# Kernel optimization log

Hardware: AMD Instinct MI355X
Metric: run time of the kernel (lower is better)

The kernel has to match this reference:

```python
import jax, jax.numpy as jnp
import numpy as np

D_MODEL = 1024
N_HEADS = 16
D_HEAD = 64


def setup_inputs() -> dict:
    key = jax.random.key(0)
    ks = jax.random.split(key, 5)
    B, T = 2, 2048
    scale = 1.0 / np.sqrt(D_MODEL)
    x = jax.random.normal(ks[0], (B, T, D_MODEL), dtype=jnp.float32)
    Wq = jax.random.normal(ks[1], (N_HEADS * D_HEAD, D_MODEL), dtype=jnp.float32) * scale
    Wk = jax.random.normal(ks[2], (N_HEADS * D_HEAD, D_MODEL), dtype=jnp.float32) * scale
    Wv = jax.random.normal(ks[3], (N_HEADS * D_HEAD, D_MODEL), dtype=jnp.float32) * scale
    Wo = jax.random.normal(ks[4], (D_MODEL, N_HEADS * D_HEAD), dtype=jnp.float32) * scale
    return {"x": x, "Wq": Wq, "Wk": Wk, "Wv": Wv, "Wo": Wo}


def reference(x, Wq, Wk, Wv, Wo):
    B, T, D = x.shape
    # Linear(y = x @ W.T), then split heads: [B, H, T, d]
    def split_heads(y):
        return y.reshape(B, T, N_HEADS, D_HEAD).transpose(0, 2, 1, 3)
    q = split_heads(x @ Wq.T)
    k = split_heads(x @ Wk.T)
    v = split_heads(x @ Wv.T)
    scale = D_HEAD ** -0.5
    # Materialized [B, H, T, T] scores, as in the original module
    scores = jnp.einsum('bhtd,bhTd->bhtT', q, k) * scale
    attn = jax.nn.softmax(scores, axis=-1)
    y = jnp.einsum('bhtT,bhTd->bhtd', attn, v)
    y = y.transpose(0, 2, 1, 3).reshape(B, T, N_HEADS * D_HEAD)
    return y @ Wo.T
```

## Files before the change

kernel.cpp:

```cpp
#include <hip/hip_runtime.h>
#include <hip/hip_bf16.h>

typedef __attribute__((ext_vector_type(8))) short bf16x8;
typedef __attribute__((ext_vector_type(4))) float f32x4;
typedef unsigned short u16t;

#define DEVINL static __device__ __forceinline__

DEVINL u16t f2bf(float f) {
  union { __hip_bfloat16 h; u16t u; } cv;
  cv.h = __float2bfloat16(f);
  return cv.u;
}

DEVINL unsigned cvt_pk_bf16(float a, float b) {
  unsigned r;
  asm("v_cvt_pk_bf16_f32 %0, %1, %2" : "=v"(r) : "v"(a), "v"(b));
  return r;
}

DEVINL void async16(void* lds, const void* g) {
  __builtin_amdgcn_global_load_lds((const __attribute__((address_space(1))) void*)g,
                                   (__attribute__((address_space(3))) void*)lds,
                                   16, 0, 0);
}

__global__ __launch_bounds__(256) void convert_bf16(
    const float* __restrict__ x,  const float* __restrict__ wq,
    const float* __restrict__ wk, const float* __restrict__ wv,
    const float* __restrict__ wo,
    u16t* __restrict__ xb, u16t* __restrict__ wqb, u16t* __restrict__ wkb,
    u16t* __restrict__ wvb, u16t* __restrict__ wob) {
  const int blk = blockIdx.x;
  const float* src; u16t* dst; size_t off;
  if (blk < 4096)      { src = x;  dst = xb;  off = (size_t)blk * 1024; }
  else if (blk < 5120) { src = wq; dst = wqb; off = (size_t)(blk - 4096) * 1024; }
  else if (blk < 6144) { src = wk; dst = wkb; off = (size_t)(blk - 5120) * 1024; }
  else if (blk < 7168) { src = wv; dst = wvb; off = (size_t)(blk - 6144) * 1024; }
  else                 { src = wo; dst = wob; off = (size_t)(blk - 7168) * 1024; }
  const size_t i = off + (size_t)threadIdx.x * 4;
  const float4 v = *(const float4*)&src[i];
  ushort4 r;
  r.x = f2bf(v.x); r.y = f2bf(v.y); r.z = f2bf(v.z); r.w = f2bf(v.w);
  *(ushort4*)&dst[i] = r;
}

template <int MODE, int BM>
__global__ __launch_bounds__(256) void gemm_bt(
    const u16t* __restrict__ A, const u16t* __restrict__ B,
    void* __restrict__ C0, void* __restrict__ C1, void* __restrict__ C2,
    int M, int N, int K) {
  constexpr int MI = BM / 32;
  __shared__ u16t As[2][BM * 32];
  __shared__ u16t Bs[2][128 * 32];

  const int tid = threadIdx.x;
  const int lane = tid & 63;
  const int w = tid >> 6;
  const int wm = w >> 1, wn = w & 1;
  const int quad = lane >> 4, cl = lane & 15;
  const int m0 = blockIdx.y * BM;
  const int n0 = blockIdx.x * 128;

  const int srow = lane >> 2;
  const int scol = (lane & 3) * 8;

  f32x4 acc[MI][4] = {};

  for (int k0 = 0; k0 < K; k0 += 64) {
    __syncthreads();
    #pragma unroll
    for (int p = 0; p < 2; ++p) {
      #pragma unroll
      for (int ii = 0; ii < BM / 64; ++ii) {
        const int c = w + ii * 4;
        async16(&As[p][c * 512], &A[(size_t)(m0 + c * 16 + srow) * K + k0 + p * 32 + scol]);
      }
      #pragma unroll
      for (int ii = 0; ii < 2; ++ii) {
        const int c = w + ii * 4;
        async16(&Bs[p][c * 512], &B[(size_t)(n0 + c * 16 + srow) * K + k0 + p * 32 + scol]);
      }
    }
    __syncthreads();
    #pragma unroll
    for (int p = 0; p < 2; ++p) {
      bf16x8 af[MI], bfr[4];
      #pragma unroll
      for (int i = 0; i < MI; ++i)
        af[i] = *(const bf16x8*)&As[p][(wm * (BM / 2) + i * 16 + cl) * 32 + quad * 8];
      #pragma unroll
      for (int j = 0; j < 4; ++j)
        bfr[j] = *(const bf16x8*)&Bs[p][(wn * 64 + j * 16 + cl) * 32 + quad * 8];
      #pragma unroll
      for (int i = 0; i < MI; ++i)
        #pragma unroll
        for (int j = 0; j < 4; ++j)
          acc[i][j] = __builtin_amdgcn_mfma_f32_16x16x32_bf16(af[i], bfr[j], acc[i][j], 0, 0, 0);
    }
  }

  const int nz = n0 >> 10;
  #pragma unroll
  for (int i = 0; i < MI; ++i)
    #pragma unroll
    for (int j = 0; j < 4; ++j) {
      const int mb = m0 + wm * (BM / 2) + i * 16 + quad * 4;
      const int n  = n0 + wn * 64 + j * 16 + cl;
      if (MODE == 0) {
        #pragma unroll
        for (int r = 0; r < 4; ++r)
          ((float*)C0)[(size_t)(mb + r) * N + n] = acc[i][j][r];
      } else {
        const int nw = n & 1023, h = nw >> 6, d = nw & 63;
        const int b = mb >> 11, tb = mb & 2047;
        const size_t bh = (size_t)(b * 16 + h);
        if (nz == 2) {
          ushort4 v4;
          v4.x = f2bf(acc[i][j][0]); v4.y = f2bf(acc[i][j][1]);
          v4.z = f2bf(acc[i][j][2]); v4.w = f2bf(acc[i][j][3]);
          const size_t addr = (bh << 17) +
              (size_t)(((d >> 4) * 256 + (tb >> 3)) * 128 + (d & 15) * 8 + (tb & 7));
          *(ushort4*)&((u16t*)C2)[addr] = v4;
        } else if (nz == 1) {
          const size_t basea = (bh << 17) +
              (size_t)(((tb >> 4) * 8 + (d >> 3)) * 128 + (d & 7));
          #pragma unroll
          for (int r = 0; r < 4; ++r)
            ((u16t*)C1)[basea + ((tb & 15) + r) * 8] = f2bf(acc[i][j][r]);
        } else {
          #pragma unroll
          for (int r = 0; r < 4; ++r)
            ((u16t*)C0)[(bh * 2048 + tb + r) * 64 + d] =
                f2bf(acc[i][j][r] * 0.18033688011112043f);
        }
      }
    }
}

__global__ __launch_bounds__(512) void flash_attn(
    const u16t* __restrict__ Q, const u16t* __restrict__ Kt,
    const u16t* __restrict__ Vt, u16t* __restrict__ Y) {
  __shared__ u16t Ps[8 * 32 * 136];
  const int tid = threadIdx.x;
  const int lane = tid & 63;
  const int w = tid >> 6;
  const int wq = w & 3;
  const int z = w >> 2;
  const int quad = lane >> 4, cl = lane & 15;
  const int bh = blockIdx.x;
  const int q0 = blockIdx.y * 128 + wq * 32;
  const u16t* Kb = Kt + ((size_t)bh << 17);
  const u16t* Vb = Vt + ((size_t)bh << 17);

  bf16x8 aq[2][2];
  #pragma unroll
  for (int h = 0; h < 2; ++h)
    #pragma unroll
    for (int ks = 0; ks < 2; ++ks)
      aq[h][ks] = *(const bf16x8*)&Q[((size_t)bh * 2048 + q0 + 16 * h + cl) * 64 + ks * 32 + quad * 8];

  bf16x8 ones8;
  #pragma unroll
  for (int i = 0; i < 8; ++i) ones8[i] = (short)0x3F80;

  f32x4 o[2][4] = {};
  f32x4 psum[2] = {};

  u16t* Pw = &Ps[w * 32 * 136];

  for (int jt = z * 8; jt < z * 8 + 8; ++jt) {
    const int j0 = jt * 128;

    f32x4 s0[8] = {}, s1[8] = {};
    #pragma unroll
    for (int ks = 0; ks < 2; ++ks) {
      bf16x8 kf[8];
      #pragma unroll
      for (int js = 0; js < 8; ++js)
        kf[js] = *(const bf16x8*)&Kb[(size_t)((((j0 >> 4) + js) * 8 + ks * 4) * 128) + lane * 8];
      #pragma unroll
      for (int js = 0; js < 8; ++js)
        s0[js] = __builtin_amdgcn_mfma_f32_16x16x32_bf16(kf[js], aq[0][ks], s0[js], 0, 0, 0);
      #pragma unroll
      for (int js = 0; js < 8; ++js)
        s1[js] = __builtin_amdgcn_mfma_f32_16x16x32_bf16(kf[js], aq[1][ks], s1[js], 0, 0, 0);
    }

    #pragma unroll
    for (int js = 0; js < 8; ++js) {
      uint2 pk0, pk1;
      pk0.x = cvt_pk_bf16(__builtin_exp2f(s0[js][0]), __builtin_exp2f(s0[js][1]));
      pk0.y = cvt_pk_bf16(__builtin_exp2f(s0[js][2]), __builtin_exp2f(s0[js][3]));
      *(uint2*)&Pw[cl * 136 + js * 16 + quad * 4] = pk0;
      pk1.x = cvt_pk_bf16(__builtin_exp2f(s1[js][0]), __builtin_exp2f(s1[js][1]));
      pk1.y = cvt_pk_bf16(__builtin_exp2f(s1[js][2]), __builtin_exp2f(s1[js][3]));
      *(uint2*)&Pw[(16 + cl) * 136 + js * 16 + quad * 4] = pk1;
    }

    #pragma unroll
    for (int ks = 0; ks < 4; ++ks) {
      const bf16x8 ap0 = *(const bf16x8*)&Pw[cl * 136 + ks * 32 + quad * 8];
      const bf16x8 ap1 = *(const bf16x8*)&Pw[(16 + cl) * 136 + ks * 32 + quad * 8];
      bf16x8 vf[4];
      #pragma unroll
      for (int ds = 0; ds < 4; ++ds)
        vf[ds] = *(const bf16x8*)&Vb[(size_t)((ds * 256 + (j0 >> 3) + ks * 4) * 128) + lane * 8];
      psum[0] = __builtin_amdgcn_mfma_f32_16x16x32_bf16(ap0, ones8, psum[0], 0, 0, 0);
      psum[1] = __builtin_amdgcn_mfma_f32_16x16x32_bf16(ap1, ones8, psum[1], 0, 0, 0);
      #pragma unroll
      for (int ds = 0; ds < 4; ++ds) {
        o[0][ds] = __builtin_amdgcn_mfma_f32_16x16x32_bf16(ap0, vf[ds], o[0][ds], 0, 0, 0);
        o[1][ds] = __builtin_amdgcn_mfma_f32_16x16x32_bf16(ap1, vf[ds], o[1][ds], 0, 0, 0);
      }
    }
  }

  if (z == 1) {
    f32x4* Po4 = (f32x4*)Pw;
    #pragma unroll
    for (int h = 0; h < 2; ++h)
      #pragma unroll
      for (int ds = 0; ds < 4; ++ds)
        Po4[(h * 4 + ds) * 64 + lane] = o[h][ds];
    f32x4* Pl4 = (f32x4*)((float*)Pw + 2048);
    if (cl == 0) {
      Pl4[quad] = psum[0];
      Pl4[4 + quad] = psum[1];
    }
  }
  __syncthreads();
  if (z == 0) {
    const float* Pp = (const float*)&Ps[(wq + 4) * 32 * 136];
    const f32x4* Qo4 = (const f32x4*)Pp;
    const f32x4* Ql4 = (const f32x4*)(Pp + 2048);
    const int b = bh >> 4, hd = bh & 15;
    #pragma unroll
    for (int h = 0; h < 2; ++h) {
      const f32x4 pt = psum[h] + Ql4[h * 4 + quad];
      float inv[4];
      #pragma unroll
      for (int r = 0; r < 4; ++r) inv[r] = __builtin_amdgcn_rcpf(pt[r]);
      #pragma unroll
      for (int ds = 0; ds < 4; ++ds) {
        const f32x4 ot = o[h][ds] + Qo4[(h * 4 + ds) * 64 + lane];
        #pragma unroll
        for (int r = 0; r < 4; ++r) {
          const int t = q0 + 16 * h + quad * 4 + r;
          const int d = ds * 16 + cl;
          Y[((size_t)b * 2048 + t) * 1024 + hd * 64 + d] = f2bf(ot[r] * inv[r]);
        }
      }
    }
  }
}

extern "C" void kernel_launch(void* const* d_in, const int* in_sizes, int n_in,
                              void* d_out, int out_size, void* d_ws, size_t ws_size,
                              hipStream_t stream) {
  (void)in_sizes; (void)n_in; (void)out_size; (void)ws_size;
  const float* x  = (const float*)d_in[0];
  const float* Wq = (const float*)d_in[1];
  const float* Wk = (const float*)d_in[2];
  const float* Wv = (const float*)d_in[3];
  const float* Wo = (const float*)d_in[4];

  char* ws = (char*)d_ws;
  const size_t MB = 1024 * 1024;
  u16t* xb  = (u16t*)(ws);
  u16t* Wqb = (u16t*)(ws + 8 * MB);
  u16t* Wkb = (u16t*)(ws + 10 * MB);
  u16t* Wvb = (u16t*)(ws + 12 * MB);
  u16t* Wob = (u16t*)(ws + 14 * MB);
  u16t* Qw  = (u16t*)(ws + 16 * MB);
  u16t* Ktw = (u16t*)(ws + 24 * MB);
  u16t* Vtw = (u16t*)(ws + 32 * MB);
  u16t* Yw  = xb;

  convert_bf16<<<8192, 256, 0, stream>>>(x, Wq, Wk, Wv, Wo, xb, Wqb, Wkb, Wvb, Wob);
  gemm_bt<1, 128><<<dim3(24, 32), 256, 0, stream>>>(
      xb, Wqb, Qw, Ktw, Vtw, 4096, 3072, 1024);
  flash_attn<<<dim3(32, 16), 512, 0, stream>>>(Qw, Ktw, Vtw, Yw);
  gemm_bt<0, 64><<<dim3(8, 64), 256, 0, stream>>>(
      Yw, Wob, d_out, d_out, d_out, 4096, 1024, 1024);
}
```

Baseline: 215.3 us.

## Drop KV-split in flash attention; batch K/V loads ahead of MFMAs

Each block now uses 4 waves instead of 8. Each wave walks all 16 key tiles, so the two half-sequence waves per query slice and their LDS reduction plus __syncthreads are gone. All K fragments and all V fragments for a tile are loaded up front, with sched_barriers, so the loads run ahead of the MFMA and exp phases. Launch bounds become (256,2) to allow two blocks per CU. The cost is higher register pressure from the preloaded fragments and half as many waves per block, which can reduce latency hiding.

```diff
diff --git a/kernel.cpp b/kernel.cpp
--- a/kernel.cpp
+++ b/kernel.cpp
@@ -138,18 +138,16 @@
     }
 }
 
-__global__ __launch_bounds__(512) void flash_attn(
+__global__ __launch_bounds__(256, 2) void flash_attn(
     const u16t* __restrict__ Q, const u16t* __restrict__ Kt,
     const u16t* __restrict__ Vt, u16t* __restrict__ Y) {
-  __shared__ u16t Ps[8 * 32 * 136];
+  __shared__ u16t Ps[4 * 32 * 136];
   const int tid = threadIdx.x;
   const int lane = tid & 63;
   const int w = tid >> 6;
-  const int wq = w & 3;
-  const int z = w >> 2;
   const int quad = lane >> 4, cl = lane & 15;
   const int bh = blockIdx.x;
-  const int q0 = blockIdx.y * 128 + wq * 32;
+  const int q0 = blockIdx.y * 128 + w * 32;
   const u16t* Kb = Kt + ((size_t)bh << 17);
   const u16t* Vb = Vt + ((size_t)bh << 17);
 
@@ -169,23 +167,35 @@
 
   u16t* Pw = &Ps[w * 32 * 136];
 
-  for (int jt = z * 8; jt < z * 8 + 8; ++jt) {
+  for (int jt = 0; jt < 16; ++jt) {
     const int j0 = jt * 128;
 
+    bf16x8 kf[2][8];
+    #pragma unroll
+    for (int ks = 0; ks < 2; ++ks)
+      #pragma unroll
+      for (int js = 0; js < 8; ++js)
+        kf[ks][js] = *(const bf16x8*)&Kb[(size_t)((((j0 >> 4) + js) * 8 + ks * 4) * 128) + lane * 8];
+    __builtin_amdgcn_sched_barrier(0);
+
     f32x4 s0[8] = {}, s1[8] = {};
     #pragma unroll
     for (int ks = 0; ks < 2; ++ks) {
-      bf16x8 kf[8];
       #pragma unroll
       for (int js = 0; js < 8; ++js)
-        kf[js] = *(const bf16x8*)&Kb[(size_t)((((j0 >> 4) + js) * 8 + ks * 4) * 128) + lane * 8];
+        s0[js] = __builtin_amdgcn_mfma_f32_16x16x32_bf16(kf[ks][js], aq[0][ks], s0[js], 0, 0, 0);
       #pragma unroll
       for (int js = 0; js < 8; ++js)
-        s0[js] = __builtin_amdgcn_mfma_f32_16x16x32_bf16(kf[js], aq[0][ks], s0[js], 0, 0, 0);
-      #pragma unroll
-      for (int js = 0; js < 8; ++js)
-        s1[js] = __builtin_amdgcn_mfma_f32_16x16x32_bf16(kf[js], aq[1][ks], s1[js], 0, 0, 0);
-    }
+        s1[js] = __builtin_amdgcn_mfma_f32_16x16x32_bf16(kf[ks][js], aq[1][ks], s1[js], 0, 0, 0);
+    }
+
+    bf16x8 vf[4][4];
+    #pragma unroll
+    for (int ks = 0; ks < 4; ++ks)
+      #pragma unroll
+      for (int ds = 0; ds < 4; ++ds)
+        vf[ks][ds] = *(const bf16x8*)&Vb[(size_t)((ds * 256 + (j0 >> 3) + ks * 4) * 128) + lane * 8];
+    __builtin_amdgcn_sched_barrier(0);
 
     #pragma unroll
     for (int js = 0; js < 8; ++js) {
@@ -202,56 +212,30 @@
     for (int ks = 0; ks < 4; ++ks) {
       const bf16x8 ap0 = *(const bf16x8*)&Pw[cl * 136 + ks * 32 + quad * 8];
       const bf16x8 ap1 = *(const bf16x8*)&Pw[(16 + cl) * 136 + ks * 32 + quad * 8];
-      bf16x8 vf[4];
-      #pragma unroll
-      for (int ds = 0; ds < 4; ++ds)
-        vf[ds] = *(const bf16x8*)&Vb[(size_t)((ds * 256 + (j0 >> 3) + ks * 4) * 128) + lane * 8];
       psum[0] = __builtin_amdgcn_mfma_f32_16x16x32_bf16(ap0, ones8, psum[0], 0, 0, 0);
       psum[1] = __builtin_amdgcn_mfma_f32_16x16x32_bf16(ap1, ones8, psum[1], 0, 0, 0);
       #pragma unroll
       for (int ds = 0; ds < 4; ++ds) {
-        o[0][ds] = __builtin_amdgcn_mfma_f32_16x16x32_bf16(ap0, vf[ds], o[0][ds], 0, 0, 0);
-        o[1][ds] = __builtin_amdgcn_mfma_f32_16x16x32_bf16(ap1, vf[ds], o[1][ds], 0, 0, 0);
+        o[0][ds] = __builtin_amdgcn_mfma_f32_16x16x32_bf16(ap0, vf[ks][ds], o[0][ds], 0, 0, 0);
+        o[1][ds] = __builtin_amdgcn_mfma_f32_16x16x32_bf16(ap1, vf[ks][ds], o[1][ds], 0, 0, 0);
       }
     }
   }
 
-  if (z == 1) {
-    f32x4* Po4 = (f32x4*)Pw;
-    #pragma unroll
-    for (int h = 0; h < 2; ++h)
-      #pragma unroll
-      for (int ds = 0; ds < 4; ++ds)
-        Po4[(h * 4 + ds) * 64 + lane] = o[h][ds];
-    f32x4* Pl4 = (f32x4*)((float*)Pw + 2048);
-    if (cl == 0) {
-      Pl4[quad] = psum[0];
-      Pl4[4 + quad] = psum[1];
-    }
-  }
-  __syncthreads();
-  if (z == 0) {
-    const float* Pp = (const float*)&Ps[(wq + 4) * 32 * 136];
-    const f32x4* Qo4 = (const f32x4*)Pp;
-    const f32x4* Ql4 = (const f32x4*)(Pp + 2048);
-    const int b = bh >> 4, hd = bh & 15;
-    #pragma unroll
-    for (int h = 0; h < 2; ++h) {
-      const f32x4 pt = psum[h] + Ql4[h * 4 + quad];
-      float inv[4];
-      #pragma unroll
-      for (int r = 0; r < 4; ++r) inv[r] = __builtin_amdgcn_rcpf(pt[r]);
-      #pragma unroll
-      for (int ds = 0; ds < 4; ++ds) {
-        const f32x4 ot = o[h][ds] + Qo4[(h * 4 + ds) * 64 + lane];
-        #pragma unroll
-        for (int r = 0; r < 4; ++r) {
-          const int t = q0 + 16 * h + quad * 4 + r;
-          const int d = ds * 16 + cl;
-          Y[((size_t)b * 2048 + t) * 1024 + hd * 64 + d] = f2bf(ot[r] * inv[r]);
-        }
-      }
-    }
+  const int b = bh >> 4, hd = bh & 15;
+  #pragma unroll
+  for (int h = 0; h < 2; ++h) {
+    float inv[4];
+    #pragma unroll
+    for (int r = 0; r < 4; ++r) inv[r] = __builtin_amdgcn_rcpf(psum[h][r]);
+    #pragma unroll
+    for (int ds = 0; ds < 4; ++ds)
+      #pragma unroll
+      for (int r = 0; r < 4; ++r) {
+        const int t = q0 + 16 * h + quad * 4 + r;
+        const int d = ds * 16 + cl;
+        Y[((size_t)b * 2048 + t) * 1024 + hd * 64 + d] = f2bf(o[h][ds][r] * inv[r]);
+      }
   }
 }
 
@@ -280,7 +264,7 @@
   convert_bf16<<<8192, 256, 0, stream>>>(x, Wq, Wk, Wv, Wo, xb, Wqb, Wkb, Wvb, Wob);
   gemm_bt<1, 128><<<dim3(24, 32), 256, 0, stream>>>(
       xb, Wqb, Qw, Ktw, Vtw, 4096, 3072, 1024);
-  flash_attn<<<dim3(32, 16), 512, 0, stream>>>(Qw, Ktw, Vtw, Yw);
+  flash_attn<<<dim3(32, 16), 256, 0, stream>>>(Qw, Ktw, Vtw, Yw);
   gemm_bt<0, 64><<<dim3(8, 64), 256, 0, stream>>>(
       Yw, Wob, d_out, d_out, d_out, 4096, 1024, 1024);
 }
```

New measurement: 191.9 us. -10.9%, faster.
